# Optimization experiments

Measured on AMD Instinct MI355X. Metric: run time of the kernel, lower is better.

The kernel has to match this reference:

```python
import jax, jax.numpy as jnp
import numpy as np

B, S, T = 4, 2048, 2048
Q_DIM = K_DIM = V_DIM = 1024
H = 8
E = V_DIM // H  # 128 per-head embed dim


def setup_inputs() -> dict:
    key = jax.random.key(0)
    ks = jax.random.split(key, 9)
    s = 0.02
    return {
        "q": jax.random.normal(ks[0], (B, S, Q_DIM), dtype=jnp.float32),
        "k": jax.random.normal(ks[1], (B, T, K_DIM), dtype=jnp.float32),
        "v": jax.random.normal(ks[2], (B, T, V_DIM), dtype=jnp.float32),
        # per-head projection weights stacked on a leading head axis
        "Wq": jax.random.normal(ks[3], (H, Q_DIM, E), dtype=jnp.float32) * s,
        "bq": jax.random.normal(ks[4], (H, E), dtype=jnp.float32) * s,
        "Wk": jax.random.normal(ks[5], (H, K_DIM, E), dtype=jnp.float32) * s,
        "bk": jax.random.normal(ks[6], (H, E), dtype=jnp.float32) * s,
        "Wv": jax.random.normal(ks[7], (H, V_DIM, E), dtype=jnp.float32) * s,
        "bv": jax.random.normal(ks[8], (H, E), dtype=jnp.float32) * s,
        "Wo": jax.random.normal(jax.random.fold_in(key, 99), (V_DIM, V_DIM), dtype=jnp.float32) * s,
    }


def reference(q, k, v, Wq, bq, Wk, bk, Wv, bv, Wo):
    # Batched per-head projections (replaces the Python loop over heads)
    qh = jnp.einsum("bsq,hqe->bhse", q, Wq) + bq[None, :, None, :]
    kh = jnp.einsum("btk,hke->bhte", k, Wk) + bk[None, :, None, :]
    vh = jnp.einsum("btv,hve->bhte", v, Wv) + bv[None, :, None, :]
    # Attention: scale is sqrt(head_dim) (ctor scale arg is overwritten)
    scores = jnp.einsum("bhse,bhte->bhst", qh, kh) / jnp.sqrt(jnp.float32(E))
    weights = 1.0 + jnp.tanh(scores)  # normalize=False branch
    heads = jnp.einsum("bhst,bhte->bhse", weights, vh)
    # concat heads along last dim: [B,S,H*E]
    merged = heads.transpose(0, 2, 1, 3).reshape(q.shape[0], q.shape[1], H * E)
    # out_layer: Linear(v_dim, v_dim, bias=False) -> x @ Wo^T
    return merged @ Wo.T
```

## Files before the change

### kernel.cpp

```cpp
#include <hip/hip_runtime.h>


using short8 = __attribute__((ext_vector_type(8))) short;
using f32x4  = __attribute__((ext_vector_type(4))) float;
typedef unsigned short u16;

struct alignas(8) us4 { u16 x, y, z, w; };

__device__ __forceinline__ u16 f2bf(float f) {
  union { float f; unsigned u; } v; v.f = f;
  return (u16)((v.u + 0x7FFFu + ((v.u >> 16) & 1u)) >> 16);
}

__device__ __forceinline__ void async16(const void* g, void* lds) {
  __builtin_amdgcn_global_load_lds(
      (const __attribute__((address_space(1))) void*)g,
      (__attribute__((address_space(3))) void*)lds, 16, 0, 0);
}

__device__ __forceinline__ f32x4 mfma16(short8 a, short8 b, f32x4 c) {
  return __builtin_amdgcn_mfma_f32_16x16x32_bf16(a, b, c, 0, 0, 0);
}

__global__ void k_cvt(const float* __restrict__ in, u16* __restrict__ out, int n4) {
  int i = blockIdx.x * blockDim.x + threadIdx.x;
  const int st = gridDim.x * blockDim.x;
  for (; i < n4; i += st) {
    float4 v = reinterpret_cast<const float4*>(in)[i];
    us4 o{f2bf(v.x), f2bf(v.y), f2bf(v.z), f2bf(v.w)};
    reinterpret_cast<us4*>(out)[i] = o;
  }
}

__global__ void k_wt(const float* __restrict__ W, u16* __restrict__ Wt) {
  __shared__ float t[32][33];
  const int k0 = blockIdx.x * 32, e0 = blockIdx.y * 32, h = blockIdx.z;
  const float* Wh = W + (size_t)h * (1024u * 128u);
  u16* Wth = Wt + (size_t)h * (128u * 1024u);
  const int c = threadIdx.x & 31, r0 = threadIdx.x >> 5;
  #pragma unroll
  for (int r = r0; r < 32; r += 8) t[r][c] = Wh[(size_t)(k0 + r) * 128 + e0 + c];
  __syncthreads();
  #pragma unroll
  for (int r = r0; r < 32; r += 8)
    Wth[(size_t)(e0 + r) * 1024 + k0 + c] = f2bf(t[c][r]);
}

template <int MODE>
__global__ __launch_bounds__(256, 3)
void k_gemm(const u16* __restrict__ A, const u16* __restrict__ W,
            const float* __restrict__ bias, void* __restrict__ outp) {
  __shared__ alignas(16) u16 As[128 * 32];
  __shared__ alignas(16) u16 Bs[128 * 32];
  const int tid = threadIdx.x;
  const int lane = tid & 63, wid = tid >> 6;
  const int wr = wid >> 1, wc = wid & 1;
  const int lr = lane & 15, lg = lane >> 4;

  const u16* Ab;
  const u16* Bb;
  const float* bp = nullptr;
  if (MODE <= 1) {
    const int bh = blockIdx.y;
    Ab = A + (size_t)(bh >> 3) * (2048u * 1024u) + (size_t)blockIdx.x * (128u * 1024u);
    Bb = W + (size_t)(bh & 7) * (128u * 1024u);
    bp = bias + (bh & 7) * 128;
  } else {
    Ab = A + (size_t)blockIdx.x * (128u * 1024u);
    Bb = W + (size_t)blockIdx.y * (128u * 1024u);
  }

  f32x4 acc[4][4] = {};

  for (int k0 = 0; k0 < 1024; k0 += 32) {
    #pragma unroll
    for (int p = 0; p < 2; ++p) {
      const int ch = p * 256 + tid;
      const int row = ch >> 2, cc = ch & 3;
      async16(Ab + (size_t)row * 1024 + k0 + cc * 8, &As[ch * 8]);
      async16(Bb + (size_t)row * 1024 + k0 + cc * 8, &Bs[ch * 8]);
    }
    __syncthreads();
    short8 a[4], b[4];
    #pragma unroll
    for (int m = 0; m < 4; ++m)
      a[m] = *(const short8*)&As[(wr * 64 + m * 16 + lr) * 32 + lg * 8];
    #pragma unroll
    for (int n = 0; n < 4; ++n)
      b[n] = *(const short8*)&Bs[(wc * 64 + n * 16 + lr) * 32 + lg * 8];
    #pragma unroll
    for (int m = 0; m < 4; ++m)
      #pragma unroll
      for (int n = 0; n < 4; ++n)
        acc[m][n] = mfma16(a[m], b[n], acc[m][n]);
    __syncthreads();
  }

  if (MODE == 0) {
    u16* O = (u16*)outp + (size_t)blockIdx.y * (2048u * 128u) + (size_t)blockIdx.x * (128u * 128u);
    #pragma unroll
    for (int n = 0; n < 4; ++n) {
      const int e = wc * 64 + n * 16 + lr;
      const float bv = bp[e];
      #pragma unroll
      for (int m = 0; m < 4; ++m) {
        const int r0 = wr * 64 + m * 16 + lg * 4;
        #pragma unroll
        for (int i = 0; i < 4; ++i)
          O[(size_t)(r0 + i) * 128 + e] = f2bf(acc[m][n][i] + bv);
      }
    }
  } else if (MODE == 1) {
    u16* O = (u16*)outp + (size_t)blockIdx.y * (128u * 2048u);
    #pragma unroll
    for (int n = 0; n < 4; ++n) {
      const int e = wc * 64 + n * 16 + lr;
      const float bv = bp[e];
      #pragma unroll
      for (int m = 0; m < 4; ++m) {
        const int t = blockIdx.x * 128 + wr * 64 + m * 16 + lg * 4;
        us4 o{f2bf(acc[m][n][0] + bv), f2bf(acc[m][n][1] + bv),
              f2bf(acc[m][n][2] + bv), f2bf(acc[m][n][3] + bv)};
        *(us4*)&O[(size_t)e * 2048 + t] = o;
      }
    }
  } else {
    float* O = (float*)outp + (size_t)blockIdx.x * (128u * 1024u) + blockIdx.y * 128;
    #pragma unroll
    for (int m = 0; m < 4; ++m)
      #pragma unroll
      for (int n = 0; n < 4; ++n)
        #pragma unroll
        for (int i = 0; i < 4; ++i)
          O[(size_t)(wr * 64 + m * 16 + lg * 4 + i) * 1024 + wc * 64 + n * 16 + lr] =
              acc[m][n][i];
  }
}

__global__ __launch_bounds__(256, 2)
void k_attn(const u16* __restrict__ QH, const u16* __restrict__ KH,
            const u16* __restrict__ VT, u16* __restrict__ MG) {
  __shared__ alignas(16) u16 Ks[64 * 128];
  __shared__ alignas(16) u16 Vs[128 * 64];
  __shared__ alignas(16) u16 Ws[128 * 64];
  const int tid = threadIdx.x, lane = tid & 63, wid = tid >> 6;
  const int lr = lane & 15, lg = lane >> 4;
  const int bh = blockIdx.y, b = bh >> 3, h = bh & 7;
  const int s0 = blockIdx.x * 128;
  const u16* Qb = QH + (size_t)bh * (2048u * 128u);
  const u16* Kb = KH + (size_t)bh * (2048u * 128u);
  const u16* Vb = VT + (size_t)bh * (128u * 2048u);

  short8 qa[2][4];
  #pragma unroll
  for (int m = 0; m < 2; ++m)
    #pragma unroll
    for (int ks = 0; ks < 4; ++ks)
      qa[m][ks] = *(const short8*)&Qb[(size_t)(s0 + wid * 32 + m * 16 + lr) * 128 + ks * 32 + lg * 8];

  f32x4 racc[2][8] = {};
  const int kx = (lr & 7) << 4;
  const float KSC = -0.25503486f;

  for (int tt = 0; tt < 32; ++tt) {
    const int t0 = tt * 64;
    #pragma unroll
    for (int p = 0; p < 4; ++p) {
      const int ch = p * 256 + tid;
      const int r = ch >> 4, cc = ch & 15;
      async16(Kb + (size_t)(t0 + r) * 128 + ((cc ^ (r & 7)) * 8), &Ks[ch * 8]);
    }
    #pragma unroll
    for (int p = 0; p < 4; ++p) {
      const int ch = p * 256 + tid;
      const int r = ch >> 3, cc = ch & 7;
      async16(Vb + (size_t)r * 2048 + t0 + ((cc ^ (r & 7)) * 8), &Vs[ch * 8]);
    }
    __syncthreads();

    f32x4 sacc[2][4] = {};
    #pragma unroll
    for (int ks = 0; ks < 4; ++ks)
      #pragma unroll
      for (int n = 0; n < 4; ++n) {
        const int krow = n * 16 + lr;
        const short8 kb =
            *(const short8*)((const char*)Ks + krow * 256 + ((ks * 64 + lg * 16) ^ kx));
        sacc[0][n] = mfma16(qa[0][ks], kb, sacc[0][n]);
        sacc[1][n] = mfma16(qa[1][ks], kb, sacc[1][n]);
      }

    #pragma unroll
    for (int m = 0; m < 2; ++m)
      #pragma unroll
      for (int n = 0; n < 4; ++n)
        #pragma unroll
        for (int i = 0; i < 4; ++i) {
          const float x = sacc[m][n][i];
          const float wv =
              2.f * __builtin_amdgcn_rcpf(1.f + __builtin_amdgcn_exp2f(x * KSC));
          const int srow = wid * 32 + m * 16 + lg * 4 + i;
          const int tcol = n * 16 + lr;
          *(u16*)((char*)Ws + srow * 128 + ((tcol * 2) ^ ((srow & 7) << 4))) = f2bf(wv);
        }

    short8 pa[2][2];
    #pragma unroll
    for (int m = 0; m < 2; ++m)
      #pragma unroll
      for (int ks = 0; ks < 2; ++ks) {
        const int prow = wid * 32 + m * 16 + lr;
        pa[m][ks] =
            *(const short8*)((const char*)Ws + prow * 128 + ((ks * 64 + lg * 16) ^ kx));
      }
    #pragma unroll
    for (int ks = 0; ks < 2; ++ks)
      #pragma unroll
      for (int n = 0; n < 8; ++n) {
        const int vrow = n * 16 + lr;
        const short8 vb =
            *(const short8*)((const char*)Vs + vrow * 128 + ((ks * 64 + lg * 16) ^ kx));
        racc[0][n] = mfma16(pa[0][ks], vb, racc[0][n]);
        racc[1][n] = mfma16(pa[1][ks], vb, racc[1][n]);
      }
    __syncthreads();
  }

  u16* Mb = MG + ((size_t)(b * 2048 + s0)) * 1024 + h * 128;
  #pragma unroll
  for (int m = 0; m < 2; ++m)
    #pragma unroll
    for (int n = 0; n < 8; ++n) {
      const int e = n * 16 + lr;
      #pragma unroll
      for (int i = 0; i < 4; ++i) {
        const int srow = wid * 32 + m * 16 + lg * 4 + i;
        Mb[(size_t)srow * 1024 + e] = f2bf(racc[m][n][i]);
      }
    }
}

extern "C" void kernel_launch(void* const* d_in, const int* in_sizes, int n_in,
                              void* d_out, int out_size, void* d_ws, size_t ws_size,
                              hipStream_t stream) {
  (void)in_sizes; (void)n_in; (void)out_size; (void)ws_size;
  const float* q  = (const float*)d_in[0];
  const float* k  = (const float*)d_in[1];
  const float* v  = (const float*)d_in[2];
  const float* Wq = (const float*)d_in[3];
  const float* bq = (const float*)d_in[4];
  const float* Wk = (const float*)d_in[5];
  const float* bk = (const float*)d_in[6];
  const float* Wv = (const float*)d_in[7];
  const float* bv = (const float*)d_in[8];
  const float* Wo = (const float*)d_in[9];

  char* ws = (char*)d_ws;
  const size_t MB16 = 16777216;
  u16* qb  = (u16*)(ws + 0 * MB16);
  u16* kb  = (u16*)(ws + 1 * MB16);
  u16* vb  = (u16*)(ws + 2 * MB16);
  u16* qh  = (u16*)(ws + 3 * MB16);
  u16* kh  = (u16*)(ws + 4 * MB16);
  u16* vT  = (u16*)(ws + 5 * MB16);
  u16* wqt = (u16*)(ws + 6 * MB16);
  u16* wkt = (u16*)(ws + 6 * MB16 + 1 * 2097152);
  u16* wvt = (u16*)(ws + 6 * MB16 + 2 * 2097152);
  u16* wob = (u16*)(ws + 6 * MB16 + 3 * 2097152);
  u16* mg  = qb;

  k_cvt<<<2048, 256, 0, stream>>>(q, qb, 2097152);
  k_cvt<<<2048, 256, 0, stream>>>(k, kb, 2097152);
  k_cvt<<<2048, 256, 0, stream>>>(v, vb, 2097152);
  k_cvt<<<1024, 256, 0, stream>>>(Wo, wob, 262144);
  k_wt<<<dim3(32, 4, 8), 256, 0, stream>>>(Wq, wqt);
  k_wt<<<dim3(32, 4, 8), 256, 0, stream>>>(Wk, wkt);
  k_wt<<<dim3(32, 4, 8), 256, 0, stream>>>(Wv, wvt);

  k_gemm<0><<<dim3(16, 32), 256, 0, stream>>>(qb, wqt, bq, qh);
  k_gemm<0><<<dim3(16, 32), 256, 0, stream>>>(kb, wkt, bk, kh);
  k_gemm<1><<<dim3(16, 32), 256, 0, stream>>>(vb, wvt, bv, vT);

  k_attn<<<dim3(16, 32), 256, 0, stream>>>(qh, kh, vT, mg);

  k_gemm<2><<<dim3(64, 8), 256, 0, stream>>>(mg, wob, nullptr, d_out);
}
```

Measured before the change: 365.8 us.

## Fuse launches, double-buffer attention, use 32x32 MFMA with register-resident weights

Merges the three input conversions, the three weight transposes and the three projection GEMMs into single launches, which cuts launch count and gives larger grids. The GEMMs move to a K-step of 64 with XOR-swizzled LDS. The attention kernel is rewritten around 32x32x16 MFMA: the score tile is computed transposed, converted to bf16 weights in registers and exchanged across half-waves by shuffles, so the LDS round trip for the weight matrix goes away. K/V tiles are double-buffered and s_setprio is added around the MFMA sections. The factor of 2 in the weights is folded into the bf16 copy of Wo, which changes rounding slightly.

```diff
diff --git a/kernel.cpp b/kernel.cpp
--- a/kernel.cpp
+++ b/kernel.cpp
@@ -3,6 +3,8 @@
 
 using short8 = __attribute__((ext_vector_type(8))) short;
 using f32x4  = __attribute__((ext_vector_type(4))) float;
+using f32x16 = __attribute__((ext_vector_type(16))) float;
+using v4i    = __attribute__((ext_vector_type(4))) int;
 typedef unsigned short u16;
 
 struct alignas(8) us4 { u16 x, y, z, w; };
@@ -10,6 +12,9 @@
 __device__ __forceinline__ u16 f2bf(float f) {
   union { float f; unsigned u; } v; v.f = f;
   return (u16)((v.u + 0x7FFFu + ((v.u >> 16) & 1u)) >> 16);
+}
+__device__ __forceinline__ unsigned packbf(float lo, float hi) {
+  return (unsigned)f2bf(lo) | ((unsigned)f2bf(hi) << 16);
 }
 
 __device__ __forceinline__ void async16(const void* g, void* lds) {
@@ -21,20 +26,43 @@
 __device__ __forceinline__ f32x4 mfma16(short8 a, short8 b, f32x4 c) {
   return __builtin_amdgcn_mfma_f32_16x16x32_bf16(a, b, c, 0, 0, 0);
 }
-
-__global__ void k_cvt(const float* __restrict__ in, u16* __restrict__ out, int n4) {
+__device__ __forceinline__ f32x16 mfma32(short8 a, short8 b, f32x16 c) {
+  return __builtin_amdgcn_mfma_f32_32x32x16_bf16(a, b, c, 0, 0, 0);
+}
+
+__global__ void k_cvt(const float* __restrict__ in, u16* __restrict__ out,
+                      int n4, float scale) {
   int i = blockIdx.x * blockDim.x + threadIdx.x;
   const int st = gridDim.x * blockDim.x;
   for (; i < n4; i += st) {
     float4 v = reinterpret_cast<const float4*>(in)[i];
+    us4 o{f2bf(v.x * scale), f2bf(v.y * scale), f2bf(v.z * scale), f2bf(v.w * scale)};
+    reinterpret_cast<us4*>(out)[i] = o;
+  }
+}
+
+__global__ void k_cvt3(const float* __restrict__ a, const float* __restrict__ b,
+                       const float* __restrict__ c, u16* __restrict__ oa,
+                       u16* __restrict__ ob, u16* __restrict__ oc) {
+  const float* in = (blockIdx.y == 0) ? a : (blockIdx.y == 1) ? b : c;
+  u16* out = (blockIdx.y == 0) ? oa : (blockIdx.y == 1) ? ob : oc;
+  int i = blockIdx.x * blockDim.x + threadIdx.x;
+  const int st = gridDim.x * blockDim.x;
+  for (; i < 2097152; i += st) {
+    float4 v = reinterpret_cast<const float4*>(in)[i];
     us4 o{f2bf(v.x), f2bf(v.y), f2bf(v.z), f2bf(v.w)};
     reinterpret_cast<us4*>(out)[i] = o;
   }
 }
 
-__global__ void k_wt(const float* __restrict__ W, u16* __restrict__ Wt) {
+__global__ void k_wt3(const float* __restrict__ Wa, const float* __restrict__ Wb,
+                      const float* __restrict__ Wc, u16* __restrict__ Ta,
+                      u16* __restrict__ Tb, u16* __restrict__ Tc) {
   __shared__ float t[32][33];
-  const int k0 = blockIdx.x * 32, e0 = blockIdx.y * 32, h = blockIdx.z;
+  const int z = blockIdx.z, h = z & 7, which = z >> 3;
+  const float* W = (which == 0) ? Wa : (which == 1) ? Wb : Wc;
+  u16* Wt = (which == 0) ? Ta : (which == 1) ? Tb : Tc;
+  const int k0 = blockIdx.x * 32, e0 = blockIdx.y * 32;
   const float* Wh = W + (size_t)h * (1024u * 128u);
   u16* Wth = Wt + (size_t)h * (128u * 1024u);
   const int c = threadIdx.x & 31, r0 = threadIdx.x >> 5;
@@ -46,197 +74,250 @@
     Wth[(size_t)(e0 + r) * 1024 + k0 + c] = f2bf(t[c][r]);
 }
 
-template <int MODE>
 __global__ __launch_bounds__(256, 3)
-void k_gemm(const u16* __restrict__ A, const u16* __restrict__ W,
-            const float* __restrict__ bias, void* __restrict__ outp) {
-  __shared__ alignas(16) u16 As[128 * 32];
-  __shared__ alignas(16) u16 Bs[128 * 32];
+void k_proj(const u16* __restrict__ qb, const u16* __restrict__ kb,
+            const u16* __restrict__ vb, const u16* __restrict__ wq,
+            const u16* __restrict__ wk, const u16* __restrict__ wv,
+            const float* __restrict__ bq, const float* __restrict__ bk,
+            const float* __restrict__ bv, u16* __restrict__ qh,
+            u16* __restrict__ kh, u16* __restrict__ vT) {
+  __shared__ alignas(16) u16 As[128 * 64];
+  __shared__ alignas(16) u16 Bs[128 * 64];
   const int tid = threadIdx.x;
   const int lane = tid & 63, wid = tid >> 6;
   const int wr = wid >> 1, wc = wid & 1;
   const int lr = lane & 15, lg = lane >> 4;
-
-  const u16* Ab;
-  const u16* Bb;
-  const float* bp = nullptr;
-  if (MODE <= 1) {
-    const int bh = blockIdx.y;
-    Ab = A + (size_t)(bh >> 3) * (2048u * 1024u) + (size_t)blockIdx.x * (128u * 1024u);
-    Bb = W + (size_t)(bh & 7) * (128u * 1024u);
-    bp = bias + (bh & 7) * 128;
-  } else {
-    Ab = A + (size_t)blockIdx.x * (128u * 1024u);
-    Bb = W + (size_t)blockIdx.y * (128u * 1024u);
-  }
+  const int y = blockIdx.y, which = y >> 5, bh = y & 31;
+
+  const u16* A = (which == 0) ? qb : (which == 1) ? kb : vb;
+  const u16* W = (which == 0) ? wq : (which == 1) ? wk : wv;
+  const float* bias = (which == 0) ? bq : (which == 1) ? bk : bv;
+  const u16* Ab = A + (size_t)(bh >> 3) * (2048u * 1024u) + (size_t)blockIdx.x * (128u * 1024u);
+  const u16* Bb = W + (size_t)(bh & 7) * (128u * 1024u);
+  const float* bp = bias + (bh & 7) * 128;
 
   f32x4 acc[4][4] = {};
-
-  for (int k0 = 0; k0 < 1024; k0 += 32) {
-    #pragma unroll
-    for (int p = 0; p < 2; ++p) {
+  const int rx = (lr & 7) << 4;
+
+  for (int k0 = 0; k0 < 1024; k0 += 64) {
+    #pragma unroll
+    for (int p = 0; p < 4; ++p) {
       const int ch = p * 256 + tid;
-      const int row = ch >> 2, cc = ch & 3;
-      async16(Ab + (size_t)row * 1024 + k0 + cc * 8, &As[ch * 8]);
-      async16(Bb + (size_t)row * 1024 + k0 + cc * 8, &Bs[ch * 8]);
-    }
-    __syncthreads();
-    short8 a[4], b[4];
-    #pragma unroll
-    for (int m = 0; m < 4; ++m)
-      a[m] = *(const short8*)&As[(wr * 64 + m * 16 + lr) * 32 + lg * 8];
-    #pragma unroll
-    for (int n = 0; n < 4; ++n)
-      b[n] = *(const short8*)&Bs[(wc * 64 + n * 16 + lr) * 32 + lg * 8];
-    #pragma unroll
-    for (int m = 0; m < 4; ++m)
+      const int r = ch >> 3, cc = ch & 7;
+      const size_t goff = (size_t)r * 1024 + k0 + ((cc ^ (r & 7)) * 8);
+      async16(Ab + goff, (char*)As + ch * 16);
+      async16(Bb + goff, (char*)Bs + ch * 16);
+    }
+    __syncthreads();
+    #pragma unroll
+    for (int kk = 0; kk < 2; ++kk) {
+      short8 a[4], b[4];
+      #pragma unroll
+      for (int m = 0; m < 4; ++m)
+        a[m] = *(const short8*)((const char*)As + (wr * 64 + m * 16 + lr) * 128 +
+                                ((kk * 64 + lg * 16) ^ rx));
       #pragma unroll
       for (int n = 0; n < 4; ++n)
-        acc[m][n] = mfma16(a[m], b[n], acc[m][n]);
-    __syncthreads();
-  }
-
-  if (MODE == 0) {
-    u16* O = (u16*)outp + (size_t)blockIdx.y * (2048u * 128u) + (size_t)blockIdx.x * (128u * 128u);
+        b[n] = *(const short8*)((const char*)Bs + (wc * 64 + n * 16 + lr) * 128 +
+                                ((kk * 64 + lg * 16) ^ rx));
+      #pragma unroll
+      for (int m = 0; m < 4; ++m)
+        #pragma unroll
+        for (int n = 0; n < 4; ++n)
+          acc[m][n] = mfma16(a[m], b[n], acc[m][n]);
+    }
+    __syncthreads();
+  }
+
+  if (which < 2) {
+    u16* O = ((which == 0) ? qh : kh) + (size_t)bh * (2048u * 128u) +
+             (size_t)blockIdx.x * (128u * 128u);
     #pragma unroll
     for (int n = 0; n < 4; ++n) {
       const int e = wc * 64 + n * 16 + lr;
-      const float bv = bp[e];
+      const float bvv = bp[e];
       #pragma unroll
       for (int m = 0; m < 4; ++m) {
         const int r0 = wr * 64 + m * 16 + lg * 4;
         #pragma unroll
         for (int i = 0; i < 4; ++i)
-          O[(size_t)(r0 + i) * 128 + e] = f2bf(acc[m][n][i] + bv);
-      }
-    }
-  } else if (MODE == 1) {
-    u16* O = (u16*)outp + (size_t)blockIdx.y * (128u * 2048u);
+          O[(size_t)(r0 + i) * 128 + e] = f2bf(acc[m][n][i] + bvv);
+      }
+    }
+  } else {
+    u16* O = vT + (size_t)bh * (128u * 2048u);
     #pragma unroll
     for (int n = 0; n < 4; ++n) {
       const int e = wc * 64 + n * 16 + lr;
-      const float bv = bp[e];
+      const float bvv = bp[e];
       #pragma unroll
       for (int m = 0; m < 4; ++m) {
         const int t = blockIdx.x * 128 + wr * 64 + m * 16 + lg * 4;
-        us4 o{f2bf(acc[m][n][0] + bv), f2bf(acc[m][n][1] + bv),
-              f2bf(acc[m][n][2] + bv), f2bf(acc[m][n][3] + bv)};
+        us4 o{f2bf(acc[m][n][0] + bvv), f2bf(acc[m][n][1] + bvv),
+              f2bf(acc[m][n][2] + bvv), f2bf(acc[m][n][3] + bvv)};
         *(us4*)&O[(size_t)e * 2048 + t] = o;
       }
     }
-  } else {
-    float* O = (float*)outp + (size_t)blockIdx.x * (128u * 1024u) + blockIdx.y * 128;
-    #pragma unroll
-    for (int m = 0; m < 4; ++m)
+  }
+}
+
+__global__ __launch_bounds__(256, 3)
+void k_gemmO(const u16* __restrict__ A, const u16* __restrict__ W,
+             float* __restrict__ O) {
+  __shared__ alignas(16) u16 As[128 * 64];
+  __shared__ alignas(16) u16 Bs[128 * 64];
+  const int tid = threadIdx.x;
+  const int lane = tid & 63, wid = tid >> 6;
+  const int wr = wid >> 1, wc = wid & 1;
+  const int lr = lane & 15, lg = lane >> 4;
+  const u16* Ab = A + (size_t)blockIdx.x * (128u * 1024u);
+  const u16* Bb = W + (size_t)blockIdx.y * (128u * 1024u);
+
+  f32x4 acc[4][4] = {};
+  const int rx = (lr & 7) << 4;
+
+  for (int k0 = 0; k0 < 1024; k0 += 64) {
+    #pragma unroll
+    for (int p = 0; p < 4; ++p) {
+      const int ch = p * 256 + tid;
+      const int r = ch >> 3, cc = ch & 7;
+      const size_t goff = (size_t)r * 1024 + k0 + ((cc ^ (r & 7)) * 8);
+      async16(Ab + goff, (char*)As + ch * 16);
+      async16(Bb + goff, (char*)Bs + ch * 16);
+    }
+    __syncthreads();
+    #pragma unroll
+    for (int kk = 0; kk < 2; ++kk) {
+      short8 a[4], b[4];
+      #pragma unroll
+      for (int m = 0; m < 4; ++m)
+        a[m] = *(const short8*)((const char*)As + (wr * 64 + m * 16 + lr) * 128 +
+                                ((kk * 64 + lg * 16) ^ rx));
       #pragma unroll
       for (int n = 0; n < 4; ++n)
+        b[n] = *(const short8*)((const char*)Bs + (wc * 64 + n * 16 + lr) * 128 +
+                                ((kk * 64 + lg * 16) ^ rx));
+      #pragma unroll
+      for (int m = 0; m < 4; ++m)
         #pragma unroll
-        for (int i = 0; i < 4; ++i)
-          O[(size_t)(wr * 64 + m * 16 + lg * 4 + i) * 1024 + wc * 64 + n * 16 + lr] =
-              acc[m][n][i];
-  }
+        for (int n = 0; n < 4; ++n)
+          acc[m][n] = mfma16(a[m], b[n], acc[m][n]);
+    }
+    __syncthreads();
+  }
+
+  float* Ob = O + (size_t)blockIdx.x * (128u * 1024u) + blockIdx.y * 128;
+  #pragma unroll
+  for (int m = 0; m < 4; ++m)
+    #pragma unroll
+    for (int n = 0; n < 4; ++n)
+      #pragma unroll
+      for (int i = 0; i < 4; ++i)
+        Ob[(size_t)(wr * 64 + m * 16 + lg * 4 + i) * 1024 + wc * 64 + n * 16 + lr] =
+            acc[m][n][i];
 }
 
 __global__ __launch_bounds__(256, 2)
 void k_attn(const u16* __restrict__ QH, const u16* __restrict__ KH,
             const u16* __restrict__ VT, u16* __restrict__ MG) {
-  __shared__ alignas(16) u16 Ks[64 * 128];
-  __shared__ alignas(16) u16 Vs[128 * 64];
-  __shared__ alignas(16) u16 Ws[128 * 64];
+  __shared__ alignas(16) u16 Ks[2][64 * 128];
+  __shared__ alignas(16) u16 Vs[2][128 * 64];
   const int tid = threadIdx.x, lane = tid & 63, wid = tid >> 6;
-  const int lr = lane & 15, lg = lane >> 4;
+  const int sl = lane & 31, hi = lane >> 5;
   const int bh = blockIdx.y, b = bh >> 3, h = bh & 7;
   const int s0 = blockIdx.x * 128;
   const u16* Qb = QH + (size_t)bh * (2048u * 128u);
   const u16* Kb = KH + (size_t)bh * (2048u * 128u);
   const u16* Vb = VT + (size_t)bh * (128u * 2048u);
-
-  short8 qa[2][4];
-  #pragma unroll
-  for (int m = 0; m < 2; ++m)
-    #pragma unroll
-    for (int ks = 0; ks < 4; ++ks)
-      qa[m][ks] = *(const short8*)&Qb[(size_t)(s0 + wid * 32 + m * 16 + lr) * 128 + ks * 32 + lg * 8];
-
-  f32x4 racc[2][8] = {};
-  const int kx = (lr & 7) << 4;
-  const float KSC = -0.25503486f;
-
-  for (int tt = 0; tt < 32; ++tt) {
-    const int t0 = tt * 64;
+  const float KSC = -0.25503473f;
+
+  short8 qf[8];
+  {
+    const u16* Qp = Qb + (size_t)(s0 + 32 * wid + sl) * 128 + hi * 8;
+    #pragma unroll
+    for (int ke = 0; ke < 8; ++ke) qf[ke] = *(const short8*)(Qp + ke * 16);
+  }
+
+  f32x16 racc[4] = {};
+  const int swr = (sl & 7) << 4;
+
+  auto STAGE = [&](int buf, int t0) {
     #pragma unroll
     for (int p = 0; p < 4; ++p) {
       const int ch = p * 256 + tid;
       const int r = ch >> 4, cc = ch & 15;
-      async16(Kb + (size_t)(t0 + r) * 128 + ((cc ^ (r & 7)) * 8), &Ks[ch * 8]);
+      async16(Kb + (size_t)(t0 + r) * 128 + ((cc ^ (r & 7)) * 8), &Ks[buf][ch * 8]);
     }
     #pragma unroll
     for (int p = 0; p < 4; ++p) {
       const int ch = p * 256 + tid;
       const int r = ch >> 3, cc = ch & 7;
-      async16(Vb + (size_t)r * 2048 + t0 + ((cc ^ (r & 7)) * 8), &Vs[ch * 8]);
-    }
-    __syncthreads();
-
-    f32x4 sacc[2][4] = {};
-    #pragma unroll
-    for (int ks = 0; ks < 4; ++ks)
-      #pragma unroll
-      for (int n = 0; n < 4; ++n) {
-        const int krow = n * 16 + lr;
-        const short8 kb =
-            *(const short8*)((const char*)Ks + krow * 256 + ((ks * 64 + lg * 16) ^ kx));
-        sacc[0][n] = mfma16(qa[0][ks], kb, sacc[0][n]);
-        sacc[1][n] = mfma16(qa[1][ks], kb, sacc[1][n]);
-      }
-
-    #pragma unroll
-    for (int m = 0; m < 2; ++m)
-      #pragma unroll
-      for (int n = 0; n < 4; ++n)
+      async16(Vb + (size_t)r * 2048 + t0 + ((cc ^ (r & 7)) * 8), &Vs[buf][ch * 8]);
+    }
+  };
+
+  STAGE(0, 0);
+  __syncthreads();
+
+  for (int tt = 0; tt < 32; ++tt) {
+    const int cur = tt & 1;
+    if (tt < 31) STAGE(cur ^ 1, (tt + 1) * 64);
+
+    const char* KsB = (const char*)Ks[cur];
+    const char* VsB = (const char*)Vs[cur];
+    #pragma unroll
+    for (int tb = 0; tb < 2; ++tb) {
+      f32x16 p = {};
+      const int krow = tb * 32 + sl;
+      __builtin_amdgcn_s_setprio(1);
+      #pragma unroll
+      for (int ke = 0; ke < 8; ++ke) {
+        const short8 kf = *(const short8*)(KsB + krow * 256 + ((ke * 32 + hi * 16) ^ swr));
+        p = mfma32(kf, qf[ke], p);
+      }
+      __builtin_amdgcn_s_setprio(0);
+
+      unsigned qpk[8];
+      #pragma unroll
+      for (int i = 0; i < 8; ++i) {
+        const float w0 = __builtin_amdgcn_rcpf(1.f + __builtin_amdgcn_exp2f(p[2 * i] * KSC));
+        const float w1 = __builtin_amdgcn_rcpf(1.f + __builtin_amdgcn_exp2f(p[2 * i + 1] * KSC));
+        qpk[i] = packbf(w0, w1);
+      }
+      unsigned o0 = __shfl_xor(qpk[0], 32), o1 = __shfl_xor(qpk[1], 32);
+      unsigned o2 = __shfl_xor(qpk[2], 32), o3 = __shfl_xor(qpk[3], 32);
+      unsigned o4 = __shfl_xor(qpk[4], 32), o5 = __shfl_xor(qpk[5], 32);
+      unsigned o6 = __shfl_xor(qpk[6], 32), o7 = __shfl_xor(qpk[7], 32);
+      union PK { v4i i; short8 s; } pk0, pk1;
+      pk0.i = (v4i){(int)(hi ? o2 : qpk[0]), (int)(hi ? o3 : qpk[1]),
+                    (int)(hi ? qpk[2] : o0), (int)(hi ? qpk[3] : o1)};
+      pk1.i = (v4i){(int)(hi ? o6 : qpk[4]), (int)(hi ? o7 : qpk[5]),
+                    (int)(hi ? qpk[6] : o4), (int)(hi ? qpk[7] : o5)};
+
+      __builtin_amdgcn_s_setprio(1);
+      #pragma unroll
+      for (int ks = 0; ks < 2; ++ks) {
+        const short8 pf = ks ? pk1.s : pk0.s;
         #pragma unroll
-        for (int i = 0; i < 4; ++i) {
-          const float x = sacc[m][n][i];
-          const float wv =
-              2.f * __builtin_amdgcn_rcpf(1.f + __builtin_amdgcn_exp2f(x * KSC));
-          const int srow = wid * 32 + m * 16 + lg * 4 + i;
-          const int tcol = n * 16 + lr;
-          *(u16*)((char*)Ws + srow * 128 + ((tcol * 2) ^ ((srow & 7) << 4))) = f2bf(wv);
+        for (int eb = 0; eb < 4; ++eb) {
+          const int vrow = eb * 32 + sl;
+          const short8 vf = *(const short8*)(
+              VsB + vrow * 128 + ((tb * 64 + ks * 32 + hi * 16) ^ swr));
+          racc[eb] = mfma32(pf, vf, racc[eb]);
         }
-
-    short8 pa[2][2];
-    #pragma unroll
-    for (int m = 0; m < 2; ++m)
-      #pragma unroll
-      for (int ks = 0; ks < 2; ++ks) {
-        const int prow = wid * 32 + m * 16 + lr;
-        pa[m][ks] =
-            *(const short8*)((const char*)Ws + prow * 128 + ((ks * 64 + lg * 16) ^ kx));
-      }
-    #pragma unroll
-    for (int ks = 0; ks < 2; ++ks)
-      #pragma unroll
-      for (int n = 0; n < 8; ++n) {
-        const int vrow = n * 16 + lr;
-        const short8 vb =
-            *(const short8*)((const char*)Vs + vrow * 128 + ((ks * 64 + lg * 16) ^ kx));
-        racc[0][n] = mfma16(pa[0][ks], vb, racc[0][n]);
-        racc[1][n] = mfma16(pa[1][ks], vb, racc[1][n]);
-      }
-    __syncthreads();
-  }
-
-  u16* Mb = MG + ((size_t)(b * 2048 + s0)) * 1024 + h * 128;
+      }
+      __builtin_amdgcn_s_setprio(0);
+    }
+    __syncthreads();
+  }
+
+  u16* Mb = MG + ((size_t)(b * 2048 + s0 + 32 * wid)) * 1024 + h * 128;
   #pragma unroll
-  for (int m = 0; m < 2; ++m)
-    #pragma unroll
-    for (int n = 0; n < 8; ++n) {
-      const int e = n * 16 + lr;
-      #pragma unroll
-      for (int i = 0; i < 4; ++i) {
-        const int srow = wid * 32 + m * 16 + lg * 4 + i;
-        Mb[(size_t)srow * 1024 + e] = f2bf(racc[m][n][i]);
-      }
+  for (int eb = 0; eb < 4; ++eb)
+    #pragma unroll
+    for (int r = 0; r < 16; ++r) {
+      const int srow = (r & 3) + 8 * (r >> 2) + 4 * hi;
+      Mb[(size_t)srow * 1024 + eb * 32 + sl] = f2bf(racc[eb][r]);
     }
 }
 
@@ -269,19 +350,14 @@
   u16* wob = (u16*)(ws + 6 * MB16 + 3 * 2097152);
   u16* mg  = qb;
 
-  k_cvt<<<2048, 256, 0, stream>>>(q, qb, 2097152);
-  k_cvt<<<2048, 256, 0, stream>>>(k, kb, 2097152);
-  k_cvt<<<2048, 256, 0, stream>>>(v, vb, 2097152);
-  k_cvt<<<1024, 256, 0, stream>>>(Wo, wob, 262144);
-  k_wt<<<dim3(32, 4, 8), 256, 0, stream>>>(Wq, wqt);
-  k_wt<<<dim3(32, 4, 8), 256, 0, stream>>>(Wk, wkt);
-  k_wt<<<dim3(32, 4, 8), 256, 0, stream>>>(Wv, wvt);
-
-  k_gemm<0><<<dim3(16, 32), 256, 0, stream>>>(qb, wqt, bq, qh);
-  k_gemm<0><<<dim3(16, 32), 256, 0, stream>>>(kb, wkt, bk, kh);
-  k_gemm<1><<<dim3(16, 32), 256, 0, stream>>>(vb, wvt, bv, vT);
+  k_cvt3<<<dim3(2048, 3), 256, 0, stream>>>(q, k, v, qb, kb, vb);
+  k_cvt<<<1024, 256, 0, stream>>>(Wo, wob, 262144, 2.0f);
+  k_wt3<<<dim3(32, 4, 24), 256, 0, stream>>>(Wq, Wk, Wv, wqt, wkt, wvt);
+
+  k_proj<<<dim3(16, 96), 256, 0, stream>>>(qb, kb, vb, wqt, wkt, wvt,
+                                           bq, bk, bv, qh, kh, vT);
 
   k_attn<<<dim3(16, 32), 256, 0, stream>>>(qh, kh, vT, mg);
 
-  k_gemm<2><<<dim3(64, 8), 256, 0, stream>>>(mg, wob, nullptr, d_out);
-}
+  k_gemmO<<<dim3(64, 8), 256, 0, stream>>>(mg, wob, (float*)d_out);
+}
```

Result: faster. 326.2 us (-10.8%).
